# Optimization experiments

Hardware: AMD Instinct MI355X
Metric: run time of the kernel (lower is better)

## Reference

```python
import jax, jax.numpy as jnp
import numpy as np

N_NODES = 50000
N_EDGES = 800000
IN_DIM = 128
HID = 256
B_SEEDS = 8192
EPS = 1e-12


def _sage_layer(h, src, dst, Wn, Ws, b):
    # mean-aggregation SAGEConv: fc_self(h) + fc_neigh(mean over in-neighbors)
    msgs = h[src]  # [E, d]
    agg = jax.ops.segment_sum(msgs, dst, num_segments=N_NODES)
    cnt = jax.ops.segment_sum(jnp.ones((src.shape[0], 1), h.dtype), dst, num_segments=N_NODES)
    neigh = agg / jnp.maximum(cnt, 1.0)
    return neigh @ Wn + h @ Ws + b


def _sage(x, src, dst, Wn1, Ws1, b1, Wn2, Ws2, b2):
    h = jax.nn.relu(_sage_layer(x, src, dst, Wn1, Ws1, b1))
    return _sage_layer(h, src, dst, Wn2, Ws2, b2)


def _l2norm(x):
    # F.normalize(p=2, dim=1)
    n = jnp.sqrt(jnp.sum(x * x, axis=1, keepdims=True))
    return x / jnp.maximum(n, EPS)


def _unique_gather(h, ids):
    # torch.unique(ids, return_inverse=True) then h[inverse]
    uniq, inv = jnp.unique(ids, return_inverse=True, size=ids.shape[0], fill_value=0)
    return h[uniq][inv]


def setup_inputs() -> dict:
    key = jax.random.key(0)
    ks = jax.random.split(key, 16)
    s = lambda d: 1.0 / np.sqrt(d)
    return {
        "x_i": jax.random.normal(ks[0], (N_NODES, IN_DIM), jnp.float32),
        "x_j": jax.random.normal(ks[1], (N_NODES, IN_DIM), jnp.float32),
        "src_i": jax.random.randint(ks[2], (N_EDGES,), 0, N_NODES, jnp.int32),
        "dst_i": jax.random.randint(ks[3], (N_EDGES,), 0, N_NODES, jnp.int32),
        "src_j": jax.random.randint(ks[4], (N_EDGES,), 0, N_NODES, jnp.int32),
        "dst_j": jax.random.randint(ks[5], (N_EDGES,), 0, N_NODES, jnp.int32),
        "ids_i": jax.random.randint(ks[6], (B_SEEDS,), 0, N_NODES, jnp.int32),
        "ids_j": jax.random.randint(ks[7], (B_SEEDS,), 0, N_NODES, jnp.int32),
        "Wn1": jax.random.normal(ks[8], (IN_DIM, HID), jnp.float32) * s(IN_DIM),
        "Ws1": jax.random.normal(ks[9], (IN_DIM, HID), jnp.float32) * s(IN_DIM),
        "b1": jnp.zeros((HID,), jnp.float32),
        "Wn2": jax.random.normal(ks[10], (HID, HID), jnp.float32) * s(HID),
        "Ws2": jax.random.normal(ks[11], (HID, HID), jnp.float32) * s(HID),
        "b2": jnp.zeros((HID,), jnp.float32),
        "W_out": jax.random.normal(ks[12], (2 * HID, 1), jnp.float32) * s(2 * HID),
        "b_out": jnp.zeros((1,), jnp.float32),
    }


def reference(x_i, x_j, src_i, dst_i, src_j, dst_j, ids_i, ids_j,
              Wn1, Ws1, b1, Wn2, Ws2, b2, W_out, b_out):
    sage_o_i = _l2norm(_sage(x_i, src_i, dst_i, Wn1, Ws1, b1, Wn2, Ws2, b2))
    sage_o_j = _l2norm(_sage(x_j, src_j, dst_j, Wn1, Ws1, b1, Wn2, Ws2, b2))
    g_i = _unique_gather(sage_o_i, ids_i)  # [B, HID]
    g_j = _unique_gather(sage_o_j, ids_j)
    h_cur = jnp.concatenate([g_i, g_j], axis=-1) @ W_out + b_out  # [B, 1]
    return jnp.stack([h_cur.squeeze(-1)])  # [1, B]
```

## Files before the change

### kernel.cpp

```cpp
#include <hip/hip_runtime.h>

constexpr int NN = 50000;
constexpr int NE = 800000;
constexpr int IND = 128;
constexpr int HD = 256;
constexpr int BS = 8192;
constexpr int NPAD = 50176;
constexpr int NBKT = 196;
constexpr int BCAP = 8192;

typedef __attribute__((ext_vector_type(8))) short short8v;
typedef __attribute__((ext_vector_type(4))) float floatx4;

__device__ inline ushort f2b(float f) {
  unsigned u = __float_as_uint(f);
  unsigned r = (u + 0x7fffu + ((u >> 16) & 1u)) >> 16;
  return (ushort)r;
}
__device__ inline float b2f(ushort b) {
  return __uint_as_float((unsigned)b << 16);
}
__device__ __forceinline__ void acc2(unsigned u, float& a0, float& a1) {
  a0 += __uint_as_float(u << 16);
  a1 += __uint_as_float(u & 0xffff0000u);
}
__device__ inline int wave_incl_scan(int x, int lane) {
#pragma unroll
  for (int d = 1; d < 64; d <<= 1) {
    int y = __shfl_up(x, d);
    if (lane >= d) x += y;
  }
  return x;
}

__device__ __forceinline__ void gload16(const ushort* g, ushort* l) {
  __builtin_amdgcn_global_load_lds(
      (const __attribute__((address_space(1))) void*)g,
      (__attribute__((address_space(3))) void*)l, 16, 0, 0);
}

__global__ __launch_bounds__(256) void k_bin_cvt(
    const float* __restrict__ Wn1, const float* __restrict__ Ws1,
    const float* __restrict__ Wn2, const float* __restrict__ Ws2,
    ushort* __restrict__ Wt, ushort* __restrict__ Whi,
    ushort* __restrict__ Wlo, const int* __restrict__ src_i,
    const int* __restrict__ dst_i, const int* __restrict__ src_j,
    const int* __restrict__ dst_j, int* __restrict__ bcnt,
    int* __restrict__ bucketbuf, const float* __restrict__ x_i,
    const float* __restrict__ x_j, ushort* __restrict__ xb2) {
  __shared__ int hist[NBKT], gbase[NBKT], lcur[NBKT];
  const int b = blockIdx.x, t = threadIdx.x;
  if (b < 256) {
    int i = b * 256 + t;
    int n = i >> 8, k = i & 255;
    float v = (k < 128) ? Wn1[k * HD + n] : Ws1[(k - 128) * HD + n];
    Wt[n * 256 + k] = f2b(v);
    return;
  }
  if (b < 768) {
    int i = (b - 256) * 256 + t;
    int n = i >> 9, k = i & 511;
    float v = (k < 256) ? Wn2[k * HD + n] : Ws2[(k - 256) * HD + n];
    ushort hi = f2b(v);
    Whi[n * 512 + k] = hi;
    Wlo[n * 512 + k] = f2b(v - b2f(hi));
    return;
  }
  if (b >= 964) {
    int i = (b - 964) * 256 + t;
    int e4 = i * 4;
    int g = e4 >= NN * IND;
    const float* xp = g ? x_j : x_i;
    float4 v = *(const float4*)(xp + (e4 - g * NN * IND));
    ushort4 u;
    u.x = f2b(v.x); u.y = f2b(v.y); u.z = f2b(v.z); u.w = f2b(v.w);
    *(ushort4*)(xb2 + e4) = u;
    return;
  }
  const int blk = b - 768;
  const int g = blk >= 98;
  const int c = blk - g * 98;
  const int* src = g ? src_j : src_i;
  const int* dst = g ? dst_j : dst_i;
  if (t < NBKT) hist[t] = 0;
  __syncthreads();
  const int e0 = c * 8192;
#pragma unroll
  for (int k = 0; k < 32; ++k) {
    int e = e0 + k * 256 + t;
    if (e < NE) atomicAdd(&hist[dst[e] >> 8], 1);
  }
  __syncthreads();
  if (t < NBKT) {
    int h = hist[t];
    gbase[t] = h ? atomicAdd(&bcnt[g * NBKT + t], h) : 0;
    lcur[t] = 0;
  }
  __syncthreads();
#pragma unroll
  for (int k = 0; k < 32; ++k) {
    int e = e0 + k * 256 + t;
    if (e < NE) {
      int d = dst[e];
      int bk = d >> 8;
      int p = gbase[bk] + atomicAdd(&lcur[bk], 1);
      if (p < BCAP)
        bucketbuf[(g * NBKT + bk) * BCAP + p] = (src[e] << 8) | (d & 255);
    }
  }
}

__global__ __launch_bounds__(256) void k_build(const int* __restrict__ bucketbuf,
                                               const int* __restrict__ bcnt,
                                               int* __restrict__ csr,
                                               int* __restrict__ cnt2,
                                               int* __restrict__ row_start2) {
  __shared__ int hist[256], lcur[256];
  __shared__ int stage[BCAP];
  __shared__ int wtv[4];
  __shared__ int carry, tot, baseSh;
  const int b = blockIdx.x;
  const int g = b >= NBKT;
  const int bb = b - g * NBKT;
  const int t = threadIdx.x, lane = t & 63;
  if (t == 0) carry = 0;
  __syncthreads();
  for (int ch = 0; ch < 2; ++ch) {
    int i = ch * 256 + t;
    int v = (i < 2 * NBKT) ? min(bcnt[i], BCAP) : 0;
    int x = wave_incl_scan(v, lane);
    if (lane == 63) wtv[t >> 6] = x;
    __syncthreads();
    if (t == 0) {
      int run = 0;
#pragma unroll
      for (int j = 0; j < 4; ++j) { int tv = wtv[j]; wtv[j] = run; run += tv; }
      tot = run;
    }
    __syncthreads();
    if (i == b) baseSh = carry + x - v + wtv[t >> 6];
    __syncthreads();
    if (t == 0) carry += tot;
    __syncthreads();
  }
  const int base = baseSh;
  const int C = min(bcnt[b], BCAP);
  const int* buf = bucketbuf + b * BCAP;
  hist[t] = 0;
  __syncthreads();
  for (int i = t; i < C; i += 256) atomicAdd(&hist[buf[i] & 255], 1);
  __syncthreads();
  int v = hist[t];
  int x = wave_incl_scan(v, lane);
  if (lane == 63) wtv[t >> 6] = x;
  __syncthreads();
  if (t == 0) {
    int run = 0;
#pragma unroll
    for (int j = 0; j < 4; ++j) { int tv = wtv[j]; wtv[j] = run; run += tv; }
  }
  __syncthreads();
  int ls = x - v + wtv[t >> 6];
  lcur[t] = ls;
  __syncthreads();
  for (int i = t; i < C; i += 256) {
    int val = buf[i];
    int p = atomicAdd(&lcur[val & 255], 1);
    stage[p] = val >> 8;
  }
  __syncthreads();
  for (int i = t; i < C; i += 256) csr[base + i] = stage[i];
  int node = bb * 256 + t;
  cnt2[g * NPAD + node] = v;
  row_start2[g * NPAD + node] = base + ls;
}

__global__ __launch_bounds__(256) void k_agg1(const ushort* __restrict__ xb2,
                                              const int* __restrict__ csr,
                                              const int* __restrict__ row_start2,
                                              const int* __restrict__ cnt2,
                                              ushort* __restrict__ aggb2) {
  int w = threadIdx.x >> 6, l = threadIdx.x & 63;
  int n = blockIdx.x * 4 + w;
  int g = n >= NN;
  int nl = n - g * NN;
  int st = row_start2[g * NPAD + nl], deg = cnt2[g * NPAD + nl];
  const ushort* xb = xb2 + g * NN * IND;
  const int h = l >> 5, c = l & 31;
  float a0 = 0.f, a1 = 0.f, a2 = 0.f, a3 = 0.f;
  int e = 0;
  for (; e + 8 <= deg; e += 8) {
    int s0 = csr[st + e + 0 + h];
    int s1 = csr[st + e + 2 + h];
    int s2 = csr[st + e + 4 + h];
    int s3 = csr[st + e + 6 + h];
    uint2 u0 = *(const uint2*)(xb + s0 * IND + c * 4);
    uint2 u1 = *(const uint2*)(xb + s1 * IND + c * 4);
    uint2 u2 = *(const uint2*)(xb + s2 * IND + c * 4);
    uint2 u3 = *(const uint2*)(xb + s3 * IND + c * 4);
    acc2(u0.x, a0, a1); acc2(u0.y, a2, a3);
    acc2(u1.x, a0, a1); acc2(u1.y, a2, a3);
    acc2(u2.x, a0, a1); acc2(u2.y, a2, a3);
    acc2(u3.x, a0, a1); acc2(u3.y, a2, a3);
  }
  for (; e + 2 <= deg; e += 2) {
    int s = csr[st + e + h];
    uint2 u = *(const uint2*)(xb + s * IND + c * 4);
    acc2(u.x, a0, a1); acc2(u.y, a2, a3);
  }
  if (e < deg && h == 0) {
    int s = csr[st + e];
    uint2 u = *(const uint2*)(xb + s * IND + c * 4);
    acc2(u.x, a0, a1); acc2(u.y, a2, a3);
  }
  a0 += __shfl_xor(a0, 32);
  a1 += __shfl_xor(a1, 32);
  a2 += __shfl_xor(a2, 32);
  a3 += __shfl_xor(a3, 32);
  if (h == 0) {
    float inv = 1.f / (float)max(deg, 1);
    ushort4 u;
    u.x = f2b(a0 * inv); u.y = f2b(a1 * inv);
    u.z = f2b(a2 * inv); u.w = f2b(a3 * inv);
    *(ushort4*)(aggb2 + (g * NN + nl) * IND + c * 4) = u;
  }
}

__global__ __launch_bounds__(256) void k_gemm1(const ushort* __restrict__ aggb2,
                                               const ushort* __restrict__ xb2,
                                               const ushort* __restrict__ Wt,
                                               const float* __restrict__ b1,
                                               ushort* __restrict__ h1b2) {
  __shared__ ushort smem[16384];
  const int t = threadIdx.x;
  const int g = blockIdx.x >= 392;
  const int row0 = (blockIdx.x - g * 392) * 128, col0 = blockIdx.y * 128;
  const ushort* aggb = aggb2 + g * NN * IND;
  const ushort* xb = xb2 + g * NN * IND;
  ushort* h1b = h1b2 + g * NN * HD;
  const int w = t >> 6, l = t & 63;
  const int wm = w & 1, wn = w >> 1;

  const int r0 = t >> 2, cs0 = t & 3;
  const int c0 = cs0 ^ (r0 & 3);
  const int rA0 = min(row0 + r0, NN - 1);
  const int rA1 = min(row0 + r0 + 64, NN - 1);
  const int gA0 = rA0 * IND + c0 * 8;
  const int gA1 = rA1 * IND + c0 * 8;
  const int gB0 = (col0 + r0) * 256 + c0 * 8;
  const int gB1 = (col0 + r0 + 64) * 256 + c0 * 8;
  const int wofs = w * 512;

  floatx4 acc[4][4];
#pragma unroll
  for (int i = 0; i < 4; ++i)
#pragma unroll
    for (int j = 0; j < 4; ++j) acc[i][j] = (floatx4){0.f, 0.f, 0.f, 0.f};

#define STAGE(buf, kk)                                                      \
  do {                                                                      \
    const ushort* Ab = ((kk) < 128) ? (aggb + (kk)) : (xb + ((kk) - 128));  \
    ushort* Ald = smem + (buf) * 4096;                                      \
    ushort* Bld = smem + 8192 + (buf) * 4096;                               \
    gload16(Ab + gA0, Ald + wofs);                                          \
    gload16(Ab + gA1, Ald + 2048 + wofs);                                   \
    gload16(Wt + gB0 + (kk), Bld + wofs);                                   \
    gload16(Wt + gB1 + (kk), Bld + 2048 + wofs);                            \
  } while (0)

  STAGE(0, 0);
  __syncthreads();
  int cur = 0;
  const int rA = l & 15, gg = l >> 4;
  for (int step = 0; step < 8; ++step) {
    if (step < 7) STAGE(cur ^ 1, (step + 1) * 32);
    const ushort* Abuf = smem + cur * 4096;
    const ushort* Bbuf = smem + 8192 + cur * 4096;
    short8v af[4], bf[4];
#pragma unroll
    for (int i = 0; i < 4; ++i) {
      int r = wm * 64 + i * 16 + rA;
      af[i] = *(const short8v*)(Abuf + r * 32 + ((gg ^ (r & 3)) * 8));
    }
#pragma unroll
    for (int j = 0; j < 4; ++j) {
      int r = wn * 64 + j * 16 + rA;
      bf[j] = *(const short8v*)(Bbuf + r * 32 + ((gg ^ (r & 3)) * 8));
    }
#pragma unroll
    for (int i = 0; i < 4; ++i)
#pragma unroll
      for (int j = 0; j < 4; ++j)
        acc[i][j] = __builtin_amdgcn_mfma_f32_16x16x32_bf16(af[i], bf[j],
                                                            acc[i][j], 0, 0, 0);
    if (step < 7) {
      __syncthreads();
      cur ^= 1;
    }
  }
#undef STAGE

  __syncthreads();
  const int rD = l >> 4, cD = l & 15;
#pragma unroll
  for (int j = 0; j < 4; ++j) {
    int cl = wn * 64 + j * 16 + cD;
    float bias = b1[col0 + cl];
#pragma unroll
    for (int i = 0; i < 4; ++i) {
      int rbase = wm * 64 + i * 16 + rD * 4;
#pragma unroll
      for (int rr = 0; rr < 4; ++rr)
        smem[(rbase + rr) * 128 + cl] = f2b(fmaxf(acc[i][j][rr] + bias, 0.f));
    }
  }
  __syncthreads();
  const int rl = t >> 4, ch = t & 15;
#pragma unroll
  for (int it = 0; it < 8; ++it) {
    int row_l = rl + it * 16;
    int grow = row0 + row_l;
    if (grow < NN)
      *(short8v*)(h1b + grow * HD + col0 + ch * 8) =
          *(const short8v*)(smem + row_l * 128 + ch * 8);
  }
}

__global__ __launch_bounds__(256) void k_agg2(
    const ushort* __restrict__ h1b2, const int* __restrict__ csr,
    const int* __restrict__ row_start2, const int* __restrict__ cnt2,
    const int* __restrict__ ids_i, const int* __restrict__ ids_j,
    ushort* __restrict__ A2) {
  __shared__ float red[4][HD];
  const int b = blockIdx.x;
  const int g = b >= BS;
  const int node = (g ? ids_j : ids_i)[b - g * BS];
  const int st = row_start2[g * NPAD + node], deg = cnt2[g * NPAD + node];
  const ushort* h1b = h1b2 + g * NN * HD;
  const int w = threadIdx.x >> 6, l = threadIdx.x & 63;
  const int h = l >> 5, c = l & 31;
  float a0 = 0.f, a1 = 0.f, a2 = 0.f, a3 = 0.f;
  float a4 = 0.f, a5 = 0.f, a6 = 0.f, a7 = 0.f;
  int e = w * 2 + h;
  for (; e + 8 < deg; e += 16) {
    int s0 = csr[st + e], s1 = csr[st + e + 8];
    uint4 u0 = *(const uint4*)(h1b + s0 * HD + c * 8);
    uint4 u1 = *(const uint4*)(h1b + s1 * HD + c * 8);
    acc2(u0.x, a0, a1); acc2(u0.y, a2, a3);
    acc2(u0.z, a4, a5); acc2(u0.w, a6, a7);
    acc2(u1.x, a0, a1); acc2(u1.y, a2, a3);
    acc2(u1.z, a4, a5); acc2(u1.w, a6, a7);
  }
  if (e < deg) {
    int s = csr[st + e];
    uint4 u = *(const uint4*)(h1b + s * HD + c * 8);
    acc2(u.x, a0, a1); acc2(u.y, a2, a3);
    acc2(u.z, a4, a5); acc2(u.w, a6, a7);
  }
  a0 += __shfl_xor(a0, 32); a1 += __shfl_xor(a1, 32);
  a2 += __shfl_xor(a2, 32); a3 += __shfl_xor(a3, 32);
  a4 += __shfl_xor(a4, 32); a5 += __shfl_xor(a5, 32);
  a6 += __shfl_xor(a6, 32); a7 += __shfl_xor(a7, 32);
  if (h == 0) {
    *(float4*)&red[w][c * 8] = (float4){a0, a1, a2, a3};
    *(float4*)&red[w][c * 8 + 4] = (float4){a4, a5, a6, a7};
  }
  __syncthreads();
  const int t = threadIdx.x;
  float s = (red[0][t] + red[1][t]) + (red[2][t] + red[3][t]);
  s *= 1.f / (float)max(deg, 1);
  A2[b * 512 + t] = f2b(s);
  A2[b * 512 + 256 + t] = h1b[node * HD + t];
}

__global__ __launch_bounds__(256) void k_head(const ushort* __restrict__ A2,
                                              const ushort* __restrict__ Whi,
                                              const ushort* __restrict__ Wlo,
                                              const float* __restrict__ b2,
                                              const float* __restrict__ W_out,
                                              float* __restrict__ outP) {
  __shared__ ushort Ahl[64 * 32];
  __shared__ ushort Bhl[256 * 32];
  __shared__ ushort Bll[256 * 32];
  __shared__ float sred[4][64][2];
  const int t = threadIdx.x;
  const int row0 = blockIdx.x * 64;
  const int w = t >> 6, l = t & 63;
  const int woff = (row0 >= BS) ? 256 : 0;
  floatx4 acc[4][4];
#pragma unroll
  for (int i = 0; i < 4; ++i)
#pragma unroll
    for (int j = 0; j < 4; ++j) acc[i][j] = (floatx4){0.f, 0.f, 0.f, 0.f};

  for (int kk = 0; kk < 512; kk += 32) {
    {
      int r = t >> 2, c = t & 3;
      int sw = (c ^ (r & 3)) * 8;
      *(short8v*)(Ahl + r * 32 + sw) =
          *(const short8v*)(A2 + (row0 + r) * 512 + kk + c * 8);
    }
#pragma unroll
    for (int s = t; s < 1024; s += 256) {
      int r = s >> 2, c = s & 3;
      int sw = (c ^ (r & 3)) * 8;
      *(short8v*)(Bhl + r * 32 + sw) =
          *(const short8v*)(Whi + r * 512 + kk + c * 8);
      *(short8v*)(Bll + r * 32 + sw) =
          *(const short8v*)(Wlo + r * 512 + kk + c * 8);
    }
    __syncthreads();
    const int rA = l & 15, gg = l >> 4;
    short8v af[4], bh[4], bl[4];
#pragma unroll
    for (int i = 0; i < 4; ++i) {
      int r = i * 16 + rA;
      af[i] = *(const short8v*)(Ahl + r * 32 + ((gg ^ (r & 3)) * 8));
    }
#pragma unroll
    for (int j = 0; j < 4; ++j) {
      int r = w * 64 + j * 16 + rA;
      int sw = (gg ^ (r & 3)) * 8;
      bh[j] = *(const short8v*)(Bhl + r * 32 + sw);
      bl[j] = *(const short8v*)(Bll + r * 32 + sw);
    }
#pragma unroll
    for (int i = 0; i < 4; ++i)
#pragma unroll
      for (int j = 0; j < 4; ++j) {
        acc[i][j] = __builtin_amdgcn_mfma_f32_16x16x32_bf16(af[i], bh[j],
                                                            acc[i][j], 0, 0, 0);
        acc[i][j] = __builtin_amdgcn_mfma_f32_16x16x32_bf16(af[i], bl[j],
                                                            acc[i][j], 0, 0, 0);
      }
    __syncthreads();
  }
  const int cD = l & 15, rD = l >> 4;
  float bj[4], wo[4];
#pragma unroll
  for (int j = 0; j < 4; ++j) {
    int col = w * 64 + j * 16 + cD;
    bj[j] = b2[col];
    wo[j] = W_out[woff + col];
  }
#pragma unroll
  for (int i = 0; i < 4; ++i)
#pragma unroll
    for (int rr = 0; rr < 4; ++rr) {
      float ssv = 0.f, dpv = 0.f;
#pragma unroll
      for (int j = 0; j < 4; ++j) {
        float v = acc[i][j][rr] + bj[j];
        ssv += v * v;
        dpv += v * wo[j];
      }
#pragma unroll
      for (int d = 1; d < 16; d <<= 1) {
        ssv += __shfl_xor(ssv, d);
        dpv += __shfl_xor(dpv, d);
      }
      if (cD == 0) {
        int row = i * 16 + rD * 4 + rr;
        sred[w][row][0] = ssv;
        sred[w][row][1] = dpv;
      }
    }
  __syncthreads();
  if (t < 64) {
    float ss = (sred[0][t][0] + sred[1][t][0]) + (sred[2][t][0] + sred[3][t][0]);
    float dp = (sred[0][t][1] + sred[1][t][1]) + (sred[2][t][1] + sred[3][t][1]);
    outP[row0 + t] = dp / fmaxf(sqrtf(ss), 1e-12f);
  }
}

__global__ __launch_bounds__(256) void k_out2(const float* __restrict__ outP,
                                              const float* __restrict__ b_out,
                                              float* __restrict__ out) {
  int s = blockIdx.x * 256 + threadIdx.x;
  if (s < BS) out[s] = outP[s] + outP[s + BS] + b_out[0];
}

extern "C" void kernel_launch(void* const* d_in, const int* in_sizes, int n_in,
                              void* d_out, int out_size, void* d_ws,
                              size_t ws_size, hipStream_t stream) {
  (void)in_sizes; (void)n_in; (void)out_size; (void)ws_size;
  const float* x_i = (const float*)d_in[0];
  const float* x_j = (const float*)d_in[1];
  const int* src_i = (const int*)d_in[2];
  const int* dst_i = (const int*)d_in[3];
  const int* src_j = (const int*)d_in[4];
  const int* dst_j = (const int*)d_in[5];
  const int* ids_i = (const int*)d_in[6];
  const int* ids_j = (const int*)d_in[7];
  const float* Wn1 = (const float*)d_in[8];
  const float* Ws1 = (const float*)d_in[9];
  const float* b1 = (const float*)d_in[10];
  const float* Wn2 = (const float*)d_in[11];
  const float* Ws2 = (const float*)d_in[12];
  const float* b2 = (const float*)d_in[13];
  const float* W_out = (const float*)d_in[14];
  const float* b_out = (const float*)d_in[15];
  float* out = (float*)d_out;

  char* w = (char*)d_ws;
  int* bcnt       = (int*)(w + 0);
  int* cnt2       = (int*)(w + 4096);
  int* row_start2 = (int*)(w + 405504);
  int* bucketbuf  = (int*)(w + 806912);
  ushort* Wt      = (ushort*)(w + 13651968);
  ushort* W2hi    = (ushort*)(w + 13783040);
  ushort* W2lo    = (ushort*)(w + 14045184);
  ushort* xb2     = (ushort*)(w + 14307328);
  ushort* aggb2   = (ushort*)(w + 39907328);
  ushort* h1b2    = (ushort*)(w + 65507328);
  int* csr        = (int*)(w + 116707328);
  ushort* A2      = (ushort*)(w + 14307328);
  float* outP     = (float*)(w + 31084544);

  hipMemsetAsync(bcnt, 0, 2 * NBKT * sizeof(int), stream);
  k_bin_cvt<<<13464, 256, 0, stream>>>(Wn1, Ws1, Wn2, Ws2, Wt, W2hi, W2lo,
                                       src_i, dst_i, src_j, dst_j, bcnt,
                                       bucketbuf, x_i, x_j, xb2);
  k_build<<<392, 256, 0, stream>>>(bucketbuf, bcnt, csr, cnt2, row_start2);
  k_agg1<<<25000, 256, 0, stream>>>(xb2, csr, row_start2, cnt2, aggb2);
  k_gemm1<<<dim3(784, 2), 256, 0, stream>>>(aggb2, xb2, Wt, b1, h1b2);
  k_agg2<<<2 * BS, 256, 0, stream>>>(h1b2, csr, row_start2, cnt2, ids_i, ids_j,
                                     A2);
  k_head<<<256, 256, 0, stream>>>(A2, W2hi, W2lo, b2, W_out, outP);
  k_out2<<<32, 256, 0, stream>>>(outP, b_out, out);
}
```

Measured before the change: 201.8 us.

## Process two nodes per wave in agg1 and widen gemm1 tile to full output

The layer-1 aggregation now assigns two consecutive nodes to each wave, with every lane loading one 4-byte bf16 pair per neighbor instead of splitting the wave into two half-wave edge streams. This halves the block count and keeps more independent gathers in flight. The first GEMM now computes all 256 output columns per block (128x256 tile, doubled shared memory and accumulators), so the A tile is loaded once instead of twice. The cost is higher register and LDS use per block, which lowers occupancy, and the two nodes in a wave can differ in degree.

```diff
diff --git a/kernel.cpp b/kernel.cpp
--- a/kernel.cpp
+++ b/kernel.cpp
@@ -181,49 +181,73 @@
                                               const int* __restrict__ cnt2,
                                               ushort* __restrict__ aggb2) {
   int w = threadIdx.x >> 6, l = threadIdx.x & 63;
-  int n = blockIdx.x * 4 + w;
-  int g = n >= NN;
-  int nl = n - g * NN;
-  int st = row_start2[g * NPAD + nl], deg = cnt2[g * NPAD + nl];
+  int p = blockIdx.x * 4 + w;
+  int nA = p * 2;
+  int g = nA >= NN;
+  int nl = nA - g * NN;
+  int base = g * NPAD + nl;
+  int stA = row_start2[base], degA = cnt2[base];
+  int stB = row_start2[base + 1], degB = cnt2[base + 1];
   const ushort* xb = xb2 + g * NN * IND;
-  const int h = l >> 5, c = l & 31;
-  float a0 = 0.f, a1 = 0.f, a2 = 0.f, a3 = 0.f;
+  float a0A = 0.f, a1A = 0.f, a0B = 0.f, a1B = 0.f;
+  int cmn = min(degA, degB);
   int e = 0;
-  for (; e + 8 <= deg; e += 8) {
-    int s0 = csr[st + e + 0 + h];
-    int s1 = csr[st + e + 2 + h];
-    int s2 = csr[st + e + 4 + h];
-    int s3 = csr[st + e + 6 + h];
-    uint2 u0 = *(const uint2*)(xb + s0 * IND + c * 4);
-    uint2 u1 = *(const uint2*)(xb + s1 * IND + c * 4);
-    uint2 u2 = *(const uint2*)(xb + s2 * IND + c * 4);
-    uint2 u3 = *(const uint2*)(xb + s3 * IND + c * 4);
-    acc2(u0.x, a0, a1); acc2(u0.y, a2, a3);
-    acc2(u1.x, a0, a1); acc2(u1.y, a2, a3);
-    acc2(u2.x, a0, a1); acc2(u2.y, a2, a3);
-    acc2(u3.x, a0, a1); acc2(u3.y, a2, a3);
-  }
-  for (; e + 2 <= deg; e += 2) {
-    int s = csr[st + e + h];
-    uint2 u = *(const uint2*)(xb + s * IND + c * 4);
-    acc2(u.x, a0, a1); acc2(u.y, a2, a3);
-  }
-  if (e < deg && h == 0) {
-    int s = csr[st + e];
-    uint2 u = *(const uint2*)(xb + s * IND + c * 4);
-    acc2(u.x, a0, a1); acc2(u.y, a2, a3);
-  }
-  a0 += __shfl_xor(a0, 32);
-  a1 += __shfl_xor(a1, 32);
-  a2 += __shfl_xor(a2, 32);
-  a3 += __shfl_xor(a3, 32);
-  if (h == 0) {
-    float inv = 1.f / (float)max(deg, 1);
-    ushort4 u;
-    u.x = f2b(a0 * inv); u.y = f2b(a1 * inv);
-    u.z = f2b(a2 * inv); u.w = f2b(a3 * inv);
-    *(ushort4*)(aggb2 + (g * NN + nl) * IND + c * 4) = u;
-  }
+  for (; e + 4 <= cmn; e += 4) {
+    int sA0 = csr[stA + e + 0], sA1 = csr[stA + e + 1];
+    int sA2 = csr[stA + e + 2], sA3 = csr[stA + e + 3];
+    int sB0 = csr[stB + e + 0], sB1 = csr[stB + e + 1];
+    int sB2 = csr[stB + e + 2], sB3 = csr[stB + e + 3];
+    unsigned uA0 = *(const unsigned*)(xb + sA0 * IND + 2 * l);
+    unsigned uA1 = *(const unsigned*)(xb + sA1 * IND + 2 * l);
+    unsigned uA2 = *(const unsigned*)(xb + sA2 * IND + 2 * l);
+    unsigned uA3 = *(const unsigned*)(xb + sA3 * IND + 2 * l);
+    unsigned uB0 = *(const unsigned*)(xb + sB0 * IND + 2 * l);
+    unsigned uB1 = *(const unsigned*)(xb + sB1 * IND + 2 * l);
+    unsigned uB2 = *(const unsigned*)(xb + sB2 * IND + 2 * l);
+    unsigned uB3 = *(const unsigned*)(xb + sB3 * IND + 2 * l);
+    acc2(uA0, a0A, a1A); acc2(uA1, a0A, a1A);
+    acc2(uA2, a0A, a1A); acc2(uA3, a0A, a1A);
+    acc2(uB0, a0B, a1B); acc2(uB1, a0B, a1B);
+    acc2(uB2, a0B, a1B); acc2(uB3, a0B, a1B);
+  }
+  int eA = e, eB = e;
+  for (; eA + 4 <= degA; eA += 4) {
+    int s0 = csr[stA + eA + 0], s1 = csr[stA + eA + 1];
+    int s2 = csr[stA + eA + 2], s3 = csr[stA + eA + 3];
+    unsigned u0 = *(const unsigned*)(xb + s0 * IND + 2 * l);
+    unsigned u1 = *(const unsigned*)(xb + s1 * IND + 2 * l);
+    unsigned u2 = *(const unsigned*)(xb + s2 * IND + 2 * l);
+    unsigned u3 = *(const unsigned*)(xb + s3 * IND + 2 * l);
+    acc2(u0, a0A, a1A); acc2(u1, a0A, a1A);
+    acc2(u2, a0A, a1A); acc2(u3, a0A, a1A);
+  }
+  for (; eA < degA; ++eA) {
+    int s = csr[stA + eA];
+    unsigned u = *(const unsigned*)(xb + s * IND + 2 * l);
+    acc2(u, a0A, a1A);
+  }
+  for (; eB + 4 <= degB; eB += 4) {
+    int s0 = csr[stB + eB + 0], s1 = csr[stB + eB + 1];
+    int s2 = csr[stB + eB + 2], s3 = csr[stB + eB + 3];
+    unsigned u0 = *(const unsigned*)(xb + s0 * IND + 2 * l);
+    unsigned u1 = *(const unsigned*)(xb + s1 * IND + 2 * l);
+    unsigned u2 = *(const unsigned*)(xb + s2 * IND + 2 * l);
+    unsigned u3 = *(const unsigned*)(xb + s3 * IND + 2 * l);
+    acc2(u0, a0B, a1B); acc2(u1, a0B, a1B);
+    acc2(u2, a0B, a1B); acc2(u3, a0B, a1B);
+  }
+  for (; eB < degB; ++eB) {
+    int s = csr[stB + eB];
+    unsigned u = *(const unsigned*)(xb + s * IND + 2 * l);
+    acc2(u, a0B, a1B);
+  }
+  float invA = 1.f / (float)max(degA, 1);
+  float invB = 1.f / (float)max(degB, 1);
+  ushort2 uA, uB;
+  uA.x = f2b(a0A * invA); uA.y = f2b(a1A * invA);
+  uB.x = f2b(a0B * invB); uB.y = f2b(a1B * invB);
+  *(ushort2*)(aggb2 + (g * NN + nl) * IND + 2 * l) = uA;
+  *(ushort2*)(aggb2 + (g * NN + nl + 1) * IND + 2 * l) = uB;
 }
 
 __global__ __launch_bounds__(256) void k_gemm1(const ushort* __restrict__ aggb2,
@@ -231,10 +255,10 @@
                                                const ushort* __restrict__ Wt,
                                                const float* __restrict__ b1,
                                                ushort* __restrict__ h1b2) {
-  __shared__ ushort smem[16384];
+  __shared__ ushort smem[32768];
   const int t = threadIdx.x;
   const int g = blockIdx.x >= 392;
-  const int row0 = (blockIdx.x - g * 392) * 128, col0 = blockIdx.y * 128;
+  const int row0 = (blockIdx.x - g * 392) * 128;
   const ushort* aggb = aggb2 + g * NN * IND;
   const ushort* xb = xb2 + g * NN * IND;
   ushort* h1b = h1b2 + g * NN * HD;
@@ -247,25 +271,29 @@
   const int rA1 = min(row0 + r0 + 64, NN - 1);
   const int gA0 = rA0 * IND + c0 * 8;
   const int gA1 = rA1 * IND + c0 * 8;
-  const int gB0 = (col0 + r0) * 256 + c0 * 8;
-  const int gB1 = (col0 + r0 + 64) * 256 + c0 * 8;
+  const int gB0 = (r0 + 0) * 256 + c0 * 8;
+  const int gB1 = (r0 + 64) * 256 + c0 * 8;
+  const int gB2 = (r0 + 128) * 256 + c0 * 8;
+  const int gB3 = (r0 + 192) * 256 + c0 * 8;
   const int wofs = w * 512;
 
-  floatx4 acc[4][4];
+  floatx4 acc[4][8];
 #pragma unroll
   for (int i = 0; i < 4; ++i)
 #pragma unroll
-    for (int j = 0; j < 4; ++j) acc[i][j] = (floatx4){0.f, 0.f, 0.f, 0.f};
+    for (int j = 0; j < 8; ++j) acc[i][j] = (floatx4){0.f, 0.f, 0.f, 0.f};
 
 #define STAGE(buf, kk)                                                      \
   do {                                                                      \
     const ushort* Ab = ((kk) < 128) ? (aggb + (kk)) : (xb + ((kk) - 128));  \
     ushort* Ald = smem + (buf) * 4096;                                      \
-    ushort* Bld = smem + 8192 + (buf) * 4096;                               \
+    ushort* Bld = smem + 8192 + (buf) * 8192;                               \
     gload16(Ab + gA0, Ald + wofs);                                          \
     gload16(Ab + gA1, Ald + 2048 + wofs);                                   \
     gload16(Wt + gB0 + (kk), Bld + wofs);                                   \
     gload16(Wt + gB1 + (kk), Bld + 2048 + wofs);                            \
+    gload16(Wt + gB2 + (kk), Bld + 4096 + wofs);                            \
+    gload16(Wt + gB3 + (kk), Bld + 6144 + wofs);                            \
   } while (0)
 
   STAGE(0, 0);
@@ -275,22 +303,22 @@
   for (int step = 0; step < 8; ++step) {
     if (step < 7) STAGE(cur ^ 1, (step + 1) * 32);
     const ushort* Abuf = smem + cur * 4096;
-    const ushort* Bbuf = smem + 8192 + cur * 4096;
-    short8v af[4], bf[4];
+    const ushort* Bbuf = smem + 8192 + cur * 8192;
+    short8v af[4], bf[8];
 #pragma unroll
     for (int i = 0; i < 4; ++i) {
       int r = wm * 64 + i * 16 + rA;
       af[i] = *(const short8v*)(Abuf + r * 32 + ((gg ^ (r & 3)) * 8));
     }
 #pragma unroll
-    for (int j = 0; j < 4; ++j) {
-      int r = wn * 64 + j * 16 + rA;
+    for (int j = 0; j < 8; ++j) {
+      int r = wn * 128 + j * 16 + rA;
       bf[j] = *(const short8v*)(Bbuf + r * 32 + ((gg ^ (r & 3)) * 8));
     }
 #pragma unroll
     for (int i = 0; i < 4; ++i)
 #pragma unroll
-      for (int j = 0; j < 4; ++j)
+      for (int j = 0; j < 8; ++j)
         acc[i][j] = __builtin_amdgcn_mfma_f32_16x16x32_bf16(af[i], bf[j],
                                                             acc[i][j], 0, 0, 0);
     if (step < 7) {
@@ -303,26 +331,26 @@
   __syncthreads();
   const int rD = l >> 4, cD = l & 15;
 #pragma unroll
-  for (int j = 0; j < 4; ++j) {
-    int cl = wn * 64 + j * 16 + cD;
-    float bias = b1[col0 + cl];
+  for (int j = 0; j < 8; ++j) {
+    int cl = wn * 128 + j * 16 + cD;
+    float bias = b1[cl];
 #pragma unroll
     for (int i = 0; i < 4; ++i) {
       int rbase = wm * 64 + i * 16 + rD * 4;
 #pragma unroll
       for (int rr = 0; rr < 4; ++rr)
-        smem[(rbase + rr) * 128 + cl] = f2b(fmaxf(acc[i][j][rr] + bias, 0.f));
-    }
-  }
-  __syncthreads();
-  const int rl = t >> 4, ch = t & 15;
-#pragma unroll
-  for (int it = 0; it < 8; ++it) {
-    int row_l = rl + it * 16;
+        smem[(rbase + rr) * 256 + cl] = f2b(fmaxf(acc[i][j][rr] + bias, 0.f));
+    }
+  }
+  __syncthreads();
+  const int rl = t >> 5, ch = t & 31;
+#pragma unroll
+  for (int it = 0; it < 16; ++it) {
+    int row_l = rl + it * 8;
     int grow = row0 + row_l;
     if (grow < NN)
-      *(short8v*)(h1b + grow * HD + col0 + ch * 8) =
-          *(const short8v*)(smem + row_l * 128 + ch * 8);
+      *(short8v*)(h1b + grow * HD + ch * 8) =
+          *(const short8v*)(smem + row_l * 256 + ch * 8);
   }
 }
 
@@ -522,8 +550,8 @@
                                        src_i, dst_i, src_j, dst_j, bcnt,
                                        bucketbuf, x_i, x_j, xb2);
   k_build<<<392, 256, 0, stream>>>(bucketbuf, bcnt, csr, cnt2, row_start2);
-  k_agg1<<<25000, 256, 0, stream>>>(xb2, csr, row_start2, cnt2, aggb2);
-  k_gemm1<<<dim3(784, 2), 256, 0, stream>>>(aggb2, xb2, Wt, b1, h1b2);
+  k_agg1<<<12500, 256, 0, stream>>>(xb2, csr, row_start2, cnt2, aggb2);
+  k_gemm1<<<784, 256, 0, stream>>>(aggb2, xb2, Wt, b1, h1b2);
   k_agg2<<<2 * BS, 256, 0, stream>>>(h1b2, csr, row_start2, cnt2, ids_i, ids_j,
                                      A2);
   k_head<<<256, 256, 0, stream>>>(A2, W2hi, W2lo, b2, W_out, outP);
```

Result: faster. 195.8 us (median of 2 runs) (-3.0%).
